# Optimization experiments

Measured on AMD Instinct MI355X. Metric: run time of the kernel, lower is better.

The kernel has to match this reference:

```python
import jax, jax.numpy as jnp
import numpy as np
from jax import lax

B, CI, CO, H, W = 8, 128, 256, 56, 56
P, K = 9, 3  # num_paths, kernel_size


def setup_inputs() -> dict:
    key = jax.random.key(0)
    ks = jax.random.split(key, 7)
    s_conv = 1.0 / np.sqrt(CI * K * K)
    s_o1 = 1.0 / np.sqrt(CI)
    s_o2 = 1.0 / np.sqrt(CO // 2)
    return {
        "x": jax.random.normal(ks[0], (B, CI, H, W), dtype=jnp.float32),
        # num_paths independent 3x3 convs, stacked on leading axis
        "kw": jax.random.uniform(ks[1], (P, CO, CI, K, K), jnp.float32, -s_conv, s_conv),
        "kb": jax.random.uniform(ks[2], (P, CO), jnp.float32, -s_conv, s_conv),
        # observer: 1x1 conv CI -> CO//2, tanh, 1x1 conv CO//2 -> P
        "ow1": jax.random.uniform(ks[3], (CO // 2, CI), jnp.float32, -s_o1, s_o1),
        "ob1": jax.random.uniform(ks[4], (CO // 2,), jnp.float32, -s_o1, s_o1),
        "ow2": jax.random.uniform(ks[5], (P, CO // 2), jnp.float32, -s_o2, s_o2),
        "ob2": jax.random.uniform(ks[6], (P,), jnp.float32, -s_o2, s_o2),
    }


def reference(x, kw, kb, ow1, ob1, ow2, ob2):
    p, co, ci, k, _ = kw.shape
    b, _, h, w = x.shape
    # All num_paths convs as a single grouped-output conv: (P*CO, CI, K, K)
    wflat = kw.reshape(p * co, ci, k, k)
    paths = lax.conv_general_dilated(
        x, wflat, window_strides=(1, 1), padding=((1, 1), (1, 1)),
        dimension_numbers=("NCHW", "OIHW", "NCHW"))
    paths = paths + kb.reshape(p * co)[None, :, None, None]
    paths = paths.reshape(b, p, co, h, w)  # [B,P,CO,H,W]

    # observer: two 1x1 convs (pure channel mixes) with tanh in between
    hmid = jnp.tanh(jnp.einsum("bchw,dc->bdhw", x, ow1) + ob1[None, :, None, None])
    scores = jnp.einsum("bdhw,pd->bphw", hmid, ow2) + ob2[None, :, None, None]

    # eval-mode collapse: argmax over paths, pixel-wise hard selection.
    # (one-hot multiply + sum over paths == gather of the winning path)
    idx = jnp.argmax(scores, axis=1)  # [B,H,W]
    out = jnp.take_along_axis(paths, idx[:, None, None, :, :], axis=1)[:, 0]  # [B,CO,H,W]
    return jax.nn.relu(out)  # norm_type='none' -> identity norm
```

## Files before the change

kernel.cpp:

```cpp
#include <hip/hip_runtime.h>
#include <hip/hip_bf16.h>


typedef unsigned int u32;

#define NPIX    25088
#define OFF_LIST 4096
#define OFF_XPAD 907264
#define OFF_W2   7796736
#define OFF_OUTP 13105152

__device__ __forceinline__ unsigned short f2bf(float f) {
  u32 u = __builtin_bit_cast(u32, f);
  u32 r = (u + 0x7FFFu + ((u >> 16) & 1u)) >> 16;
  return (unsigned short)r;
}
__device__ __forceinline__ float bflo(u32 w) {
  return __builtin_bit_cast(float, w << 16);
}
__device__ __forceinline__ float bfhi(u32 w) {
  return __builtin_bit_cast(float, w & 0xFFFF0000u);
}

#define GLDS16(g, l)                                                        \
  __builtin_amdgcn_global_load_lds(                                         \
      (const __attribute__((address_space(1))) u32*)(g),                    \
      (__attribute__((address_space(3))) u32*)(l), 16, 0, 0)
#define GLDS4(g, l)                                                         \
  __builtin_amdgcn_global_load_lds(                                         \
      (const __attribute__((address_space(1))) u32*)(g),                    \
      (__attribute__((address_space(3))) u32*)(l), 4, 0, 0)

typedef __attribute__((ext_vector_type(8))) short bf16x8;
typedef __attribute__((ext_vector_type(4))) float f32x4;

__global__ __launch_bounds__(512) void k_front(
    const float* __restrict__ x, const float* __restrict__ kw,
    const float* __restrict__ ow1, const float* __restrict__ ob1,
    const float* __restrict__ ow2, const float* __restrict__ ob2,
    u32* __restrict__ xpad, u32* __restrict__ w2,
    int* __restrict__ cnt, int* __restrict__ list) {
  __shared__ __attribute__((aligned(16))) char smraw[32768];
  __shared__ int lcnt[9], lbase[9];

  int bid = blockIdx.x;
  int tid = threadIdx.x;
  int ln = tid & 63, wv = tid >> 6;

  if (bid < 392) {
    float* xs  = (float*)smraw;
    float* red = (float*)smraw;
    int dgu = __builtin_amdgcn_readfirstlane(wv);
    int pix0 = bid * 64;
    int b = pix0 / 3136, s0 = pix0 - b * 3136;
    int pix = pix0 + ln;
    const float* xsrc = x + (size_t)b * 401408 + s0 + ln;

#pragma unroll
    for (int r = 0; r < 16; ++r) {
      int row = dgu * 16 + r;
      GLDS4(xsrc + (size_t)row * 3136, &xs[row * 64 + ln]);
    }

    if (tid < 9) lcnt[tid] = 0;

    float h[16];
    const float* o1 = ob1 + dgu * 16;
#pragma unroll
    for (int i = 0; i < 16; ++i) h[i] = o1[i];
    const float* w1b = ow1 + dgu * 16 * 128;

    __syncthreads();

    for (int c = 0; c < 16; ++c) {
      float xc[8];
#pragma unroll
      for (int j = 0; j < 8; ++j) xc[j] = xs[(c * 8 + j) * 64 + ln];
#pragma unroll
      for (int i = 0; i < 16; ++i) {
        const float* wr = w1b + i * 128 + c * 8;
        float a = h[i];
#pragma unroll
        for (int j = 0; j < 8; ++j) a = fmaf(wr[j], xc[j], a);
        h[i] = a;
      }
    }
    __syncthreads();

#pragma unroll
    for (int i = 0; i < 16; ++i) h[i] = tanhf(h[i]);

#pragma unroll
    for (int p = 0; p < 9; ++p) {
      float sc = 0.f;
      const float* wr = ow2 + p * 128 + dgu * 16;
#pragma unroll
      for (int i = 0; i < 16; ++i) sc = fmaf(wr[i], h[i], sc);
      red[wv * 576 + ln * 9 + p] = sc;
    }
    __syncthreads();

    int bi = 0, slot = 0;
    if (wv == 0) {
      float best = 0.f;
#pragma unroll
      for (int p = 0; p < 9; ++p) {
        float v = ob2[p];
#pragma unroll
        for (int g = 0; g < 8; ++g) v += red[g * 576 + ln * 9 + p];
        if (p == 0 || v > best) { best = v; bi = p; }
      }
      slot = atomicAdd(&lcnt[bi], 1);
    }
    __syncthreads();
    if (tid < 9) lbase[tid] = atomicAdd(&cnt[tid], lcnt[tid]);
    __syncthreads();
    if (wv == 0) list[bi * NPIX + lbase[bi] + slot] = pix;

  } else if (bid < 840) {
    u32* xt = (u32*)smraw;
    int bh = bid - 392;
    int b = bh / 56, hh = bh - b * 56;
    const float* xr = x + (size_t)b * 401408 + hh * 56;
#pragma unroll
    for (int r = 0; r < 8; ++r) {
      int ci = wv * 16 + 2 * r;
      if (ln < 56) {
        float f0 = xr[(size_t)ci * 3136 + ln];
        float f1 = xr[(size_t)(ci + 1) * 3136 + ln];
        xt[ln * 65 + (ci >> 1)] = (u32)f2bf(f0) | ((u32)f2bf(f1) << 16);
      }
    }
    __syncthreads();
    u32* orow = xpad + (size_t)(b * 58 + hh + 1) * 58 * 64;
    for (int w = wv; w < 56; w += 8)
      orow[(w + 1) * 64 + ln] = xt[w * 65 + ln];
    if (wv == 0) orow[ln] = 0;
    else if (wv == 1) orow[57 * 64 + ln] = 0;
    if (hh == 0) {
      u32* hrow = xpad + (size_t)(b * 58) * 58 * 64;
      for (int i = tid; i < 58 * 64; i += 512) hrow[i] = 0;
    } else if (hh == 55) {
      u32* hrow = xpad + (size_t)(b * 58 + 57) * 58 * 64;
      for (int i = tid; i < 58 * 64; i += 512) hrow[i] = 0;
    }

  } else {
    float* kt = (float*)smraw;
    int base = (bid - 840) * 4;
    const float* src = kw + (size_t)base * 1152;
#pragma unroll
    for (int i = 0; i < 9; ++i) kt[i * 512 + tid] = src[i * 512 + tid];
    __syncthreads();
    for (int t = tid; t < 2304; t += 512) {
      int pl = t / 576, d = t - pl * 576;
      int tap = d >> 6, cp = d & 63;
      float v0 = kt[pl * 1152 + 18 * cp + tap];
      float v1 = kt[pl * 1152 + 18 * cp + 9 + tap];
      w2[(size_t)(base + pl) * 576 + d] = (u32)f2bf(v0) | ((u32)f2bf(v1) << 16);
    }
  }
}

__global__ __launch_bounds__(256, 4) void k_conv(
    const int* __restrict__ cnt, const int* __restrict__ list,
    const char* __restrict__ xpadB, const char* __restrict__ w2B,
    const float* __restrict__ kb, unsigned short* __restrict__ outp) {
  __shared__ short Wlds[2][4096];
  __shared__ short Plds[2][2048];
  __shared__ int offsB[64], pixSB[64];
  __shared__ float kbl[128];

  int bid = blockIdx.x;
  int half = bid & 1, tb = bid >> 1;
  int p = -1, cntp = 0;
  for (int pp = 0; pp < 9; ++pp) {
    int c = cnt[pp];
    int tt = (c + 63) >> 6;
    if (p < 0) {
      if (tb < tt) { p = pp; cntp = c; }
      else tb -= tt;
    }
  }
  if (p < 0) return;
  int nbase = tb * 64;
  int tid = threadIdx.x;

  if (tid < 64) {
    int g = nbase + tid;
    int pixid = list[p * NPIX + (g < cntp ? g : nbase)];
    int b = pixid / 3136, s = pixid - b * 3136;
    int h = s / 56, w = s - h * 56;
    offsB[tid] = ((b * 58 + h) * 58 + w) * 256;
    pixSB[tid] = pixid;
  }
  if (tid < 128) kbl[tid] = kb[p * 256 + half * 128 + tid];
  __syncthreads();

  int segsw = ((tid & 3) ^ ((tid >> 3) & 3)) * 16;
  int na = tid >> 2;
  int offP = offsB[na] + segsw;
  const char* wrow = w2B + (size_t)(p * 256 + half * 128) * 2304;
  const char* wp0 = wrow + (size_t)na * 2304 + segsw;
  const char* wp1 = wrow + (size_t)(64 + na) * 2304 + segsw;

  auto stage = [&](int c, int q) {
    int tap = c >> 2, kc = c & 3;
    int wko = tap * 256 + kc * 64;
    int tapoff = ((tap / 3) * 58 + (tap % 3)) * 256 + kc * 64;
    GLDS16(wp0 + wko, &Wlds[q][tid * 8]);
    GLDS16(wp1 + wko, &Wlds[q][2048 + tid * 8]);
    GLDS16(xpadB + (size_t)(offP + tapoff), &Plds[q][tid * 8]);
  };

  f32x4 acc[4][2];
#pragma unroll
  for (int mt = 0; mt < 4; ++mt)
#pragma unroll
    for (int nt = 0; nt < 2; ++nt) acc[mt][nt] = (f32x4)0.f;

  int lane = tid & 63, wave = tid >> 6;
  int wm = wave >> 1, wn = wave & 1;
  int l15 = lane & 15, quad = lane >> 4;
  int slot = (quad ^ ((l15 >> 1) & 3)) * 8;
  int mrow = wm * 64 + l15;
  int nrow = wn * 32 + l15;

  stage(0, 0);
  for (int c = 0; c < 36; ++c) {
    __syncthreads();
    if (c + 1 < 36) stage(c + 1, (c + 1) & 1);
    int q = c & 1;
    bf16x8 af[4], bfr[2];
#pragma unroll
    for (int mt = 0; mt < 4; ++mt)
      af[mt] = *(const bf16x8*)&Wlds[q][(mrow + mt * 16) * 32 + slot];
#pragma unroll
    for (int nt = 0; nt < 2; ++nt)
      bfr[nt] = *(const bf16x8*)&Plds[q][(nrow + nt * 16) * 32 + slot];
#pragma unroll
    for (int mt = 0; mt < 4; ++mt)
#pragma unroll
      for (int nt = 0; nt < 2; ++nt)
        acc[mt][nt] = __builtin_amdgcn_mfma_f32_16x16x32_bf16(
            af[mt], bfr[nt], acc[mt][nt], 0, 0, 0);
  }

#pragma unroll
  for (int nt = 0; nt < 2; ++nt) {
    int n = wn * 32 + nt * 16 + l15;
    if ((nbase + n) >= cntp) continue;
    size_t rowb = (size_t)pixSB[n] * 256 + half * 128;
#pragma unroll
    for (int mt = 0; mt < 4; ++mt) {
      int co0 = wm * 64 + mt * 16 + quad * 4;
      float v0 = acc[mt][nt][0] + kbl[co0 + 0];
      float v1 = acc[mt][nt][1] + kbl[co0 + 1];
      float v2 = acc[mt][nt][2] + kbl[co0 + 2];
      float v3 = acc[mt][nt][3] + kbl[co0 + 3];
      v0 = v0 > 0.f ? v0 : 0.f;  v1 = v1 > 0.f ? v1 : 0.f;
      v2 = v2 > 0.f ? v2 : 0.f;  v3 = v3 > 0.f ? v3 : 0.f;
      u32 lo = (u32)f2bf(v0) | ((u32)f2bf(v1) << 16);
      u32 hi = (u32)f2bf(v2) | ((u32)f2bf(v3) << 16);
      *(u32*)&outp[rowb + co0]     = lo;
      *(u32*)&outp[rowb + co0 + 2] = hi;
    }
  }
}

__global__ __launch_bounds__(256) void k_out(
    const u32* __restrict__ outp, float* __restrict__ out) {
  __shared__ u32 t[64 * 129];
  int tid = threadIdx.x;
  int pix0 = blockIdx.x * 64;
  const u32* src = outp + (size_t)pix0 * 128;
  for (int i = tid; i < 8192; i += 256)
    t[(i >> 7) * 129 + (i & 127)] = src[i];
  __syncthreads();

  int ln = tid & 63, coq = tid >> 6;
  int b = pix0 / 3136, s = pix0 - b * 3136 + ln;
  float* dst = out + (size_t)b * 802816 + s;
  const u32* row = &t[ln * 129 + coq * 32];
#pragma unroll
  for (int j = 0; j < 32; ++j) {
    u32 w = row[j];
    int co = 2 * (coq * 32 + j);
    dst[(size_t)co * 3136]       = bflo(w);
    dst[(size_t)(co + 1) * 3136] = bfhi(w);
  }
}

extern "C" void kernel_launch(void* const* d_in, const int* in_sizes, int n_in,
                              void* d_out, int out_size, void* d_ws, size_t ws_size,
                              hipStream_t stream) {
  const float* x   = (const float*)d_in[0];
  const float* kw  = (const float*)d_in[1];
  const float* kb  = (const float*)d_in[2];
  const float* ow1 = (const float*)d_in[3];
  const float* ob1 = (const float*)d_in[4];
  const float* ow2 = (const float*)d_in[5];
  const float* ob2 = (const float*)d_in[6];
  float* out = (float*)d_out;
  char* ws = (char*)d_ws;

  int* cnt  = (int*)(ws);
  int* list = (int*)(ws + OFF_LIST);
  u32* xpad = (u32*)(ws + OFF_XPAD);
  u32* w2   = (u32*)(ws + OFF_W2);
  unsigned short* outp = (unsigned short*)(ws + OFF_OUTP);

  hipMemsetAsync(cnt, 0, 64, stream);

  k_front<<<1416, 512, 0, stream>>>(x, kw, ow1, ob1, ow2, ob2, xpad, w2,
                                    cnt, list);
  k_conv<<<802, 256, 0, stream>>>(cnt, list, (const char*)xpad, (const char*)w2,
                                  kb, outp);
  k_out<<<392, 256, 0, stream>>>((const u32*)outp, out);
}
```

Measured before the change: 157.2 us.

## Split conv K-loop across two blocks and reduce partials in output kernel

The implicit-GEMM conv's 36 K-chunks are split into two ranges (20 and 16 chunks) handled by separate blocks, doubling the grid. Each block writes a bf16 partial sum to its own slab of the workspace, with bias added only in the first slab. The transpose kernel now reads both slabs, adds them, applies ReLU and writes fp32 NCHW output. Launch bounds are raised to 6 waves per SIMD. The aim is more blocks per CU to hide latency, at the cost of twice the intermediate write and read traffic and an extra bf16 rounding of the partial sums.

Result: slower. 165.2 us (+5.1%).

```diff
diff --git a/kernel.cpp b/kernel.cpp
--- a/kernel.cpp
+++ b/kernel.cpp
@@ -162,7 +162,7 @@
   }
 }
 
-__global__ __launch_bounds__(256, 4) void k_conv(
+__global__ __launch_bounds__(256, 6) void k_conv(
     const int* __restrict__ cnt, const int* __restrict__ list,
     const char* __restrict__ xpadB, const char* __restrict__ w2B,
     const float* __restrict__ kb, unsigned short* __restrict__ outp) {
@@ -172,7 +172,8 @@
   __shared__ float kbl[128];
 
   int bid = blockIdx.x;
-  int half = bid & 1, tb = bid >> 1;
+  int kh = bid & 1;
+  int half = (bid >> 1) & 1, tb = bid >> 2;
   int p = -1, cntp = 0;
   for (int pp = 0; pp < 9; ++pp) {
     int c = cnt[pp];
@@ -194,7 +195,7 @@
     offsB[tid] = ((b * 58 + h) * 58 + w) * 256;
     pixSB[tid] = pixid;
   }
-  if (tid < 128) kbl[tid] = kb[p * 256 + half * 128 + tid];
+  if (tid < 128) kbl[tid] = (kh == 0) ? kb[p * 256 + half * 128 + tid] : 0.f;
   __syncthreads();
 
   int segsw = ((tid & 3) ^ ((tid >> 3) & 3)) * 16;
@@ -226,11 +227,13 @@
   int mrow = wm * 64 + l15;
   int nrow = wn * 32 + l15;
 
-  stage(0, 0);
-  for (int c = 0; c < 36; ++c) {
-    __syncthreads();
-    if (c + 1 < 36) stage(c + 1, (c + 1) & 1);
-    int q = c & 1;
+  int c0 = kh ? 20 : 0;
+  int cN = kh ? 16 : 20;
+  stage(c0, 0);
+  for (int i = 0; i < cN; ++i) {
+    __syncthreads();
+    if (i + 1 < cN) stage(c0 + i + 1, (i + 1) & 1);
+    int q = i & 1;
     bf16x8 af[4], bfr[2];
 #pragma unroll
     for (int mt = 0; mt < 4; ++mt)
@@ -250,7 +253,7 @@
   for (int nt = 0; nt < 2; ++nt) {
     int n = wn * 32 + nt * 16 + l15;
     if ((nbase + n) >= cntp) continue;
-    size_t rowb = (size_t)pixSB[n] * 256 + half * 128;
+    size_t rowb = (size_t)(kh * NPIX + pixSB[n]) * 256 + half * 128;
 #pragma unroll
     for (int mt = 0; mt < 4; ++mt) {
       int co0 = wm * 64 + mt * 16 + quad * 4;
@@ -258,8 +261,6 @@
       float v1 = acc[mt][nt][1] + kbl[co0 + 1];
       float v2 = acc[mt][nt][2] + kbl[co0 + 2];
       float v3 = acc[mt][nt][3] + kbl[co0 + 3];
-      v0 = v0 > 0.f ? v0 : 0.f;  v1 = v1 > 0.f ? v1 : 0.f;
-      v2 = v2 > 0.f ? v2 : 0.f;  v3 = v3 > 0.f ? v3 : 0.f;
       u32 lo = (u32)f2bf(v0) | ((u32)f2bf(v1) << 16);
       u32 hi = (u32)f2bf(v2) | ((u32)f2bf(v3) << 16);
       *(u32*)&outp[rowb + co0]     = lo;
@@ -270,24 +271,33 @@
 
 __global__ __launch_bounds__(256) void k_out(
     const u32* __restrict__ outp, float* __restrict__ out) {
-  __shared__ u32 t[64 * 129];
+  __shared__ u32 t[2][64 * 65];
   int tid = threadIdx.x;
-  int pix0 = blockIdx.x * 64;
-  const u32* src = outp + (size_t)pix0 * 128;
-  for (int i = tid; i < 8192; i += 256)
-    t[(i >> 7) * 129 + (i & 127)] = src[i];
+  int hb = blockIdx.x & 1;
+  int pix0 = (blockIdx.x >> 1) * 64;
+#pragma unroll
+  for (int kh = 0; kh < 2; ++kh) {
+    const u32* src = outp + ((size_t)(kh * NPIX + pix0) * 128) + hb * 64;
+    for (int i = tid; i < 4096; i += 256)
+      t[kh][(i >> 6) * 65 + (i & 63)] = src[(i >> 6) * 128 + (i & 63)];
+  }
   __syncthreads();
 
   int ln = tid & 63, coq = tid >> 6;
   int b = pix0 / 3136, s = pix0 - b * 3136 + ln;
   float* dst = out + (size_t)b * 802816 + s;
-  const u32* row = &t[ln * 129 + coq * 32];
-#pragma unroll
-  for (int j = 0; j < 32; ++j) {
-    u32 w = row[j];
-    int co = 2 * (coq * 32 + j);
-    dst[(size_t)co * 3136]       = bflo(w);
-    dst[(size_t)(co + 1) * 3136] = bfhi(w);
+#pragma unroll
+  for (int j = 0; j < 16; ++j) {
+    int dw = coq * 16 + j;
+    u32 w0 = t[0][ln * 65 + dw];
+    u32 w1 = t[1][ln * 65 + dw];
+    float v0 = bflo(w0) + bflo(w1);
+    float v1 = bfhi(w0) + bfhi(w1);
+    v0 = v0 > 0.f ? v0 : 0.f;
+    v1 = v1 > 0.f ? v1 : 0.f;
+    int co = hb * 128 + 2 * dw;
+    dst[(size_t)co * 3136]       = v0;
+    dst[(size_t)(co + 1) * 3136] = v1;
   }
 }
 
@@ -314,7 +324,7 @@
 
   k_front<<<1416, 512, 0, stream>>>(x, kw, ow1, ob1, ow2, ob2, xpad, w2,
                                     cnt, list);
-  k_conv<<<802, 256, 0, stream>>>(cnt, list, (const char*)xpad, (const char*)w2,
-                                  kb, outp);
-  k_out<<<392, 256, 0, stream>>>((const u32*)outp, out);
-}
+  k_conv<<<1604, 256, 0, stream>>>(cnt, list, (const char*)xpad, (const char*)w2,
+                                   kb, outp);
+  k_out<<<784, 256, 0, stream>>>((const u32*)outp, out);
+}
```
